# Kernel optimization log

Hardware: AMD Instinct MI355X
Metric: run time of the kernel (lower is better)

The kernel has to match this reference:

```python
import jax, jax.numpy as jnp
import numpy as np

B, N, M = 4, 1024, 1024
PFD, AD, GFD = 1024, 256, 512
H, DH = 4, 64
NR, CUT = 16, 2.0
SCALE = DH ** -0.5
OFFSETS = jnp.linspace(0.0, CUT, NR)
COEFF = -0.5 / (CUT / (NR - 1)) ** 2


def _ln(x, g, b, eps=1e-5):
    mu = x.mean(-1, keepdims=True)
    var = ((x - mu) ** 2).mean(-1, keepdims=True)
    return (x - mu) / jnp.sqrt(var + eps) * g + b


def _kabsch(src, tgt, w):
    # weighted Kabsch: rotation/translation aligning src -> tgt
    w = w / (w.sum(-1, keepdims=True) + 1e-8)  # (B,N)
    cs = jnp.einsum('bn,bnc->bc', w, src)
    ct = jnp.einsum('bn,bnc->bc', w, tgt)
    sc = src - cs[:, None]
    tc = tgt - ct[:, None]
    Hm = jnp.einsum('bn,bnc,bnd->bcd', w, sc, tc)  # (B,3,3)
    U, _, Vt = jnp.linalg.svd(Hm)
    V = jnp.swapaxes(Vt, -1, -2)
    d = jnp.linalg.det(V @ jnp.swapaxes(U, -1, -2))
    D = jnp.stack([jnp.ones_like(d), jnp.ones_like(d), d], -1)  # (B,3)
    R = jnp.einsum('bij,bj,bkj->bik', V, D, U)
    t = ct - jnp.einsum('bij,bj->bi', R, cs)
    return R, t


def setup_inputs():
    key = jax.random.key(0)
    it = iter(jax.random.split(key, 48))
    nrm = lambda s, sc=1.0: jax.random.normal(next(it), s, jnp.float32) * sc
    return {
        'src_point_feats': nrm((B, N, PFD)),
        'tgt_point_feats': nrm((B, M, PFD)),
        'src_points': nrm((B, N, 3)),
        'tgt_points': nrm((B, M, 3)),
        'tgt_global': nrm((B, GFD)),
        'sfp_w': nrm((PFD, AD), 0.02), 'sfp_b': jnp.zeros((AD,)), 'sfp_g': jnp.ones((AD,)), 'sfp_bb': jnp.zeros((AD,)),
        'tfp_w': nrm((PFD, AD), 0.02), 'tfp_b': jnp.zeros((AD,)), 'tfp_g': jnp.ones((AD,)), 'tfp_bb': jnp.zeros((AD,)),
        'rbf_w': nrm((NR, H), 0.1),
        'qw': nrm((AD, AD), 0.02), 'qb': jnp.zeros((AD,)),
        'kw': nrm((AD, AD), 0.02), 'kb': jnp.zeros((AD,)),
        'vw': nrm((AD, AD), 0.02), 'vb': jnp.zeros((AD,)),
        'ow': nrm((AD, AD), 0.02), 'ob': jnp.zeros((AD,)),
        'n1_g': jnp.ones((AD,)), 'n1_b': jnp.zeros((AD,)),
        'f1_w': nrm((AD, 4 * AD), 0.02), 'f1_b': jnp.zeros((4 * AD,)),
        'f2_w': nrm((4 * AD, AD), 0.02), 'f2_b': jnp.zeros((AD,)),
        'n2_g': jnp.ones((AD,)), 'n2_b': jnp.zeros((AD,)),
        'scp_w': nrm((AD, AD), 0.02), 'scp_b': jnp.zeros((AD,)),
        'tcp_w': nrm((AD, AD), 0.02), 'tcp_b': jnp.zeros((AD,)),
        'temperature': jnp.array(0.05, jnp.float32),
        'gp_w': nrm((AD, GFD), 0.02), 'gp_b': jnp.zeros((GFD,)), 'gp_g': jnp.ones((GFD,)), 'gp_bb': jnp.zeros((GFD,)),
    }


def reference(src_point_feats, tgt_point_feats, src_points, tgt_points, tgt_global,
              sfp_w, sfp_b, sfp_g, sfp_bb, tfp_w, tfp_b, tfp_g, tfp_bb, rbf_w,
              qw, qb, kw, kb, vw, vb, ow, ob, n1_g, n1_b,
              f1_w, f1_b, f2_w, f2_b, n2_g, n2_b,
              scp_w, scp_b, tcp_w, tcp_b, temperature,
              gp_w, gp_b, gp_g, gp_bb):
    # feature projections
    src_proj = jax.nn.relu(_ln(src_point_feats @ sfp_w + sfp_b, sfp_g, sfp_bb))  # (B,N,AD)
    tgt_proj = jax.nn.relu(_ln(tgt_point_feats @ tfp_w + tfp_b, tfp_g, tfp_bb))  # (B,M,AD)
    # inter-cloud geometric bias: cdist -> gaussian RBF -> per-head linear (dist no-grad)
    d2 = ((src_points ** 2).sum(-1)[:, :, None] + (tgt_points ** 2).sum(-1)[:, None, :]
          - 2.0 * jnp.einsum('bnc,bmc->bnm', src_points, tgt_points))
    dist = jnp.sqrt(jnp.clip(d2, 0.0))  # (B,N,M)
    rbf = jnp.exp(COEFF * (dist[..., None] - OFFSETS) ** 2)  # (B,N,M,NR)
    rbf = jax.lax.stop_gradient(rbf)
    bias = jnp.einsum('bnmr,rh->bhnm', rbf, rbf_w)
    # cross attention with geo bias (pre-LN on both streams, shared LN params)
    xq = _ln(src_proj, n1_g, n1_b)
    xc = _ln(tgt_proj, n1_g, n1_b)
    q = (xq @ qw + qb).reshape(B, N, H, DH)
    k = (xc @ kw + kb).reshape(B, M, H, DH)
    v = (xc @ vw + vb).reshape(B, M, H, DH)
    logits = jnp.einsum('bnhd,bmhd->bhnm', q, k) * SCALE + bias
    p = jax.nn.softmax(logits, axis=-1)
    attn_out = jnp.einsum('bhnm,bmhd->bnhd', p, v).reshape(B, N, AD) @ ow + ob
    x = src_proj + attn_out
    # FFN block (exact GELU as in torch)
    h = _ln(x, n2_g, n2_b)
    x = x + (jax.nn.gelu(h @ f1_w + f1_b, approximate=False) @ f2_w + f2_b)
    # soft correspondences + 3-step log-domain Sinkhorn
    src_corr = x @ scp_w + scp_b
    tgt_corr = tgt_proj @ tcp_w + tcp_b
    tau = jnp.clip(temperature, 0.01, 1.0)
    logS = jnp.einsum('bnd,bmd->bnm', src_corr, tgt_corr) / tau
    for _ in range(3):
        logS = logS - jax.nn.logsumexp(logS, axis=-1, keepdims=True)
        logS = logS - jax.nn.logsumexp(logS, axis=-2, keepdims=True)
    S = jnp.exp(logS)
    tgt_corr_points = jnp.einsum('bnm,bmc->bnc', S, tgt_points)
    confidence = S.max(-1)
    R_res, t_res = _kabsch(src_points, tgt_corr_points, confidence)
    src_global_new = jax.nn.relu(_ln(x.max(1) @ gp_w + gp_b, gp_g, gp_bb))
    combined = jnp.concatenate([src_global_new, tgt_global], axis=-1)
    return R_res, t_res, combined, confidence, S
```

## Files before the change

### kernel.cpp

```cpp
#include <hip/hip_runtime.h>
#include <hip/hip_bf16.h>
#include <math.h>

constexpr int Bn  = 4;
constexpr int Nn  = 1024;
constexpr int Mmm = 1024;
constexpr int PFDc = 1024;
constexpr int ADc  = 256;
constexpr int GFDc = 512;
constexpr int Hc   = 4;
constexpr int NRc  = 16;
constexpr int NSPLIT = 32;
constexpr float COEFFc = -28.125f;
constexpr float SCALEc = 0.125f;
constexpr float STEPc  = 2.0f / 15.0f;

__device__ __forceinline__ float addf(float a, float b) { return a + b; }
__device__ __forceinline__ double addd(double a, double b) { return a + b; }

#define BLK_REDUCE_F(OP, VAR, RES) \
  red[tid] = (VAR); __syncthreads(); \
  for (int st_ = 128; st_ > 0; st_ >>= 1) { if (tid < st_) red[tid] = OP(red[tid], red[tid + st_]); __syncthreads(); } \
  (RES) = red[0]; __syncthreads();

#define BLK_REDUCE_D(OP, VAR, RES) \
  redd[tid] = (VAR); __syncthreads(); \
  for (int st_ = 128; st_ > 0; st_ >>= 1) { if (tid < st_) redd[tid] = OP(redd[tid], redd[tid + st_]); __syncthreads(); } \
  (RES) = redd[0]; __syncthreads();

__global__ __launch_bounds__(256) void gemm_k(
    const float* __restrict__ A, const float* __restrict__ W, const float* __restrict__ bias,
    const float* __restrict__ addsrc, float* __restrict__ C,
    int R, int K, int Cc, int act)
{
  __shared__ __align__(16) float As[16][68];
  __shared__ __align__(16) float Ws[16][68];
  const int tid = threadIdx.x;
  const int tx = tid & 15, ty = tid >> 4;
  const int r0 = blockIdx.y * 64, c0 = blockIdx.x * 64;
  float acc[4][4] = {};
  for (int k0 = 0; k0 < K; k0 += 16) {
    #pragma unroll
    for (int j = 0; j < 4; ++j) {
      int e = tid + j * 256;
      int ar = e >> 4, ak = e & 15;
      int gr = r0 + ar;
      As[ak][ar] = (gr < R) ? A[(size_t)gr * K + k0 + ak] : 0.f;
    }
    #pragma unroll
    for (int j = 0; j < 4; ++j) {
      int e = tid + j * 256;
      int wk = e >> 6, wc = e & 63;
      int gc = c0 + wc;
      Ws[wk][wc] = (gc < Cc) ? W[(size_t)(k0 + wk) * Cc + gc] : 0.f;
    }
    __syncthreads();
    #pragma unroll
    for (int kk = 0; kk < 16; ++kk) {
      float4 av = *(const float4*)&As[kk][ty * 4];
      float4 wv = *(const float4*)&Ws[kk][tx * 4];
      float a[4] = {av.x, av.y, av.z, av.w};
      float w[4] = {wv.x, wv.y, wv.z, wv.w};
      #pragma unroll
      for (int i = 0; i < 4; ++i)
        #pragma unroll
        for (int j = 0; j < 4; ++j)
          acc[i][j] = fmaf(a[i], w[j], acc[i][j]);
    }
    __syncthreads();
  }
  #pragma unroll
  for (int i = 0; i < 4; ++i) {
    int r = r0 + ty * 4 + i;
    if (r >= R) continue;
    #pragma unroll
    for (int j = 0; j < 4; ++j) {
      int c = c0 + tx * 4 + j;
      if (c >= Cc) continue;
      float v = acc[i][j] + bias[c];
      if (addsrc) v += addsrc[(size_t)r * Cc + c];
      if (act == 1) v = 0.5f * v * (1.f + erff(v * 0.70710678118654752f));
      C[(size_t)r * Cc + c] = v;
    }
  }
}

__global__ __launch_bounds__(256) void gemm256_k(
    const float* __restrict__ A, const float* __restrict__ W, const float* __restrict__ bias,
    const float* __restrict__ addsrc, float* __restrict__ C,
    int R, int K, int Cc, int act)
{
  __shared__ __align__(16) float As[2][16][68];
  __shared__ __align__(16) float Ws[2][16][68];
  const int tid = threadIdx.x;
  const int tx = tid & 15, ty = tid >> 4;
  const int r0 = blockIdx.y * 64, c0 = blockIdx.x * 64;
  float acc[4][4] = {};
  float ra[4], rb[4];

  #pragma unroll
  for (int j = 0; j < 4; ++j) {
    int e = tid + j * 256;
    ra[j] = A[(size_t)(r0 + (e >> 4)) * K + (e & 15)];
    rb[j] = W[(size_t)(e >> 6) * Cc + c0 + (e & 63)];
  }
  #pragma unroll
  for (int j = 0; j < 4; ++j) {
    int e = tid + j * 256;
    As[0][e & 15][e >> 4] = ra[j];
    Ws[0][e >> 6][e & 63] = rb[j];
  }
  __syncthreads();

  const int nstep = K >> 4;
  for (int s = 0; s < nstep; ++s) {
    const int cur = s & 1;
    if (s + 1 < nstep) {
      const int k0 = (s + 1) << 4;
      #pragma unroll
      for (int j = 0; j < 4; ++j) {
        int e = tid + j * 256;
        ra[j] = A[(size_t)(r0 + (e >> 4)) * K + k0 + (e & 15)];
        rb[j] = W[(size_t)(k0 + (e >> 6)) * Cc + c0 + (e & 63)];
      }
    }
    #pragma unroll
    for (int kk = 0; kk < 16; ++kk) {
      float4 av = *(const float4*)&As[cur][kk][ty * 4];
      float4 wv = *(const float4*)&Ws[cur][kk][tx * 4];
      float a[4] = {av.x, av.y, av.z, av.w};
      float w[4] = {wv.x, wv.y, wv.z, wv.w};
      #pragma unroll
      for (int i = 0; i < 4; ++i)
        #pragma unroll
        for (int j = 0; j < 4; ++j)
          acc[i][j] = fmaf(a[i], w[j], acc[i][j]);
    }
    if (s + 1 < nstep) {
      #pragma unroll
      for (int j = 0; j < 4; ++j) {
        int e = tid + j * 256;
        As[cur ^ 1][e & 15][e >> 4] = ra[j];
        Ws[cur ^ 1][e >> 6][e & 63] = rb[j];
      }
    }
    __syncthreads();
  }
  #pragma unroll
  for (int i = 0; i < 4; ++i) {
    int r = r0 + ty * 4 + i;
    #pragma unroll
    for (int j = 0; j < 4; ++j) {
      int c = c0 + tx * 4 + j;
      float v = acc[i][j] + bias[c];
      if (addsrc) v += addsrc[(size_t)r * Cc + c];
      if (act == 1) v = 0.5f * v * (1.f + erff(v * 0.70710678118654752f));
      C[(size_t)r * Cc + c] = v;
    }
  }
}

__global__ __launch_bounds__(256) void gemm_sk_k(
    const float* __restrict__ A, const float* __restrict__ W, float* __restrict__ P)
{
  __shared__ __align__(16) float As[2][16][68];
  __shared__ __align__(16) float Ws[2][16][68];
  const int tid = threadIdx.x;
  const int tx = tid & 15, ty = tid >> 4;
  const int r0 = blockIdx.y * 64, c0 = blockIdx.x * 64;
  const int koff = blockIdx.z * 256;
  float acc[4][4] = {};
  float ra[4], rb[4];

  #pragma unroll
  for (int j = 0; j < 4; ++j) {
    int e = tid + j * 256;
    ra[j] = A[(size_t)(r0 + (e >> 4)) * 1024 + koff + (e & 15)];
    rb[j] = W[(size_t)(koff + (e >> 6)) * 256 + c0 + (e & 63)];
  }
  #pragma unroll
  for (int j = 0; j < 4; ++j) {
    int e = tid + j * 256;
    As[0][e & 15][e >> 4] = ra[j];
    Ws[0][e >> 6][e & 63] = rb[j];
  }
  __syncthreads();

  for (int s = 0; s < 16; ++s) {
    const int cur = s & 1;
    if (s + 1 < 16) {
      const int k0 = koff + ((s + 1) << 4);
      #pragma unroll
      for (int j = 0; j < 4; ++j) {
        int e = tid + j * 256;
        ra[j] = A[(size_t)(r0 + (e >> 4)) * 1024 + k0 + (e & 15)];
        rb[j] = W[(size_t)(k0 + (e >> 6)) * 256 + c0 + (e & 63)];
      }
    }
    #pragma unroll
    for (int kk = 0; kk < 16; ++kk) {
      float4 av = *(const float4*)&As[cur][kk][ty * 4];
      float4 wv = *(const float4*)&Ws[cur][kk][tx * 4];
      float a[4] = {av.x, av.y, av.z, av.w};
      float w[4] = {wv.x, wv.y, wv.z, wv.w};
      #pragma unroll
      for (int i = 0; i < 4; ++i)
        #pragma unroll
        for (int j = 0; j < 4; ++j)
          acc[i][j] = fmaf(a[i], w[j], acc[i][j]);
    }
    if (s + 1 < 16) {
      #pragma unroll
      for (int j = 0; j < 4; ++j) {
        int e = tid + j * 256;
        As[cur ^ 1][e & 15][e >> 4] = ra[j];
        Ws[cur ^ 1][e >> 6][e & 63] = rb[j];
      }
    }
    __syncthreads();
  }
  float* Pz = P + (size_t)blockIdx.z * 1048576;
  #pragma unroll
  for (int i = 0; i < 4; ++i) {
    int r = r0 + ty * 4 + i;
    #pragma unroll
    for (int j = 0; j < 4; ++j)
      Pz[(size_t)r * 256 + c0 + tx * 4 + j] = acc[i][j];
  }
}

__global__ __launch_bounds__(256) void ln4_k(
    const float* __restrict__ p, const float* __restrict__ bias,
    const float* __restrict__ g, const float* __restrict__ bb,
    float* __restrict__ out, int relu)
{
  const int row = blockIdx.x;
  const int tid = threadIdx.x;
  size_t o = (size_t)row * 256 + tid;
  float x = p[o] + p[o + 1048576] + p[o + 2097152] + p[o + 3145728] + bias[tid];
  float s = x, s2 = x * x;
  #pragma unroll
  for (int off = 32; off > 0; off >>= 1) {
    s  += __shfl_xor(s, off, 64);
    s2 += __shfl_xor(s2, off, 64);
  }
  __shared__ float as_[4], as2_[4];
  const int wv = tid >> 6, ln = tid & 63;
  if (ln == 0) { as_[wv] = s; as2_[wv] = s2; }
  __syncthreads();
  s  = as_[0] + as_[1] + as_[2] + as_[3];
  s2 = as2_[0] + as2_[1] + as2_[2] + as2_[3];
  float mu = s * (1.f / 256.f);
  float var = fmaxf(s2 * (1.f / 256.f) - mu * mu, 0.f);
  float inv = 1.f / sqrtf(var + 1e-5f);
  float v = (x - mu) * inv * g[tid] + bb[tid];
  if (relu) v = fmaxf(v, 0.f);
  out[o] = v;
}

__global__ __launch_bounds__(256) void red4_k(
    const float* __restrict__ p, const float* __restrict__ bias, float* __restrict__ out)
{
  size_t i = (size_t)blockIdx.x * 256 + threadIdx.x;
  out[i] += p[i] + p[i + 1048576] + p[i + 2097152] + p[i + 3145728] + bias[threadIdx.x];
}

__global__ __launch_bounds__(256) void pack_kv_k(
    const float* __restrict__ kw, const float* __restrict__ kb,
    const float* __restrict__ vw, const float* __restrict__ vb,
    float* __restrict__ kvw, float* __restrict__ kvb)
{
  int i = blockIdx.x * 256 + threadIdx.x;
  if (i < 256 * 512) {
    int r = i >> 9, c = i & 511;
    kvw[i] = (c < 256) ? kw[r * 256 + c] : vw[r * 256 + (c - 256)];
  } else if (i < 256 * 512 + 512) {
    int c = i - 256 * 512;
    kvb[c] = (c < 256) ? kb[c] : vb[c - 256];
  }
}

__global__ __launch_bounds__(256) void gemm_nt256_k(
    const float* __restrict__ A, const float* __restrict__ Bm, float* __restrict__ C,
    const float* __restrict__ temp)
{
  const int K = ADc;
  __shared__ __align__(16) float As[2][16][68];
  __shared__ __align__(16) float Bs[2][16][68];
  const int tid = threadIdx.x;
  const int tx = tid & 15, ty = tid >> 4;
  const int b = blockIdx.z;
  const int r0 = blockIdx.y * 64, c0 = blockIdx.x * 64;
  const float* Ab = A + (size_t)b * Nn * K;
  const float* Bb = Bm + (size_t)b * Mmm * K;
  float* Cb = C + (size_t)b * Nn * Mmm;
  float tau = fminf(fmaxf(temp[0], 0.01f), 1.0f);
  float inv_tau = 1.f / tau;
  float acc[4][4] = {};
  float ra[4], rb[4];

  #pragma unroll
  for (int j = 0; j < 4; ++j) {
    int e = tid + j * 256;
    ra[j] = Ab[(size_t)(r0 + (e >> 4)) * K + (e & 15)];
    rb[j] = Bb[(size_t)(c0 + (e >> 4)) * K + (e & 15)];
  }
  #pragma unroll
  for (int j = 0; j < 4; ++j) {
    int e = tid + j * 256;
    As[0][e & 15][e >> 4] = ra[j];
    Bs[0][e & 15][e >> 4] = rb[j];
  }
  __syncthreads();

  for (int s = 0; s < 16; ++s) {
    const int cur = s & 1;
    if (s + 1 < 16) {
      const int k0 = (s + 1) << 4;
      #pragma unroll
      for (int j = 0; j < 4; ++j) {
        int e = tid + j * 256;
        ra[j] = Ab[(size_t)(r0 + (e >> 4)) * K + k0 + (e & 15)];
        rb[j] = Bb[(size_t)(c0 + (e >> 4)) * K + k0 + (e & 15)];
      }
    }
    #pragma unroll
    for (int kk = 0; kk < 16; ++kk) {
      float4 av = *(const float4*)&As[cur][kk][ty * 4];
      float4 wv = *(const float4*)&Bs[cur][kk][tx * 4];
      float a[4] = {av.x, av.y, av.z, av.w};
      float w[4] = {wv.x, wv.y, wv.z, wv.w};
      #pragma unroll
      for (int i = 0; i < 4; ++i)
        #pragma unroll
        for (int j = 0; j < 4; ++j)
          acc[i][j] = fmaf(a[i], w[j], acc[i][j]);
    }
    if (s + 1 < 16) {
      #pragma unroll
      for (int j = 0; j < 4; ++j) {
        int e = tid + j * 256;
        As[cur ^ 1][e & 15][e >> 4] = ra[j];
        Bs[cur ^ 1][e & 15][e >> 4] = rb[j];
      }
    }
    __syncthreads();
  }
  #pragma unroll
  for (int i = 0; i < 4; ++i) {
    int r = r0 + ty * 4 + i;
    #pragma unroll
    for (int j = 0; j < 4; ++j) {
      int c = c0 + tx * 4 + j;
      Cb[(size_t)r * Mmm + c] = acc[i][j] * inv_tau;
    }
  }
}

__global__ __launch_bounds__(256) void ln_k(
    const float* __restrict__ in, const float* __restrict__ g, const float* __restrict__ bb,
    float* __restrict__ out, int Cc, int relu)
{
  const int tid = threadIdx.x;
  const int row = blockIdx.x;
  const float* x = in + (size_t)row * Cc;
  float* o = out + (size_t)row * Cc;
  __shared__ float red[256];
  float s = 0.f;
  for (int j = tid; j < Cc; j += 256) s += x[j];
  float tot; BLK_REDUCE_F(addf, s, tot);
  float mu = tot / Cc;
  float s2 = 0.f;
  for (int j = tid; j < Cc; j += 256) { float d = x[j] - mu; s2 += d * d; }
  float tot2; BLK_REDUCE_F(addf, s2, tot2);
  float inv = 1.f / sqrtf(tot2 / Cc + 1e-5f);
  for (int j = tid; j < Cc; j += 256) {
    float v = (x[j] - mu) * inv * g[j] + bb[j];
    if (relu) v = fmaxf(v, 0.f);
    o[j] = v;
  }
}

__global__ __launch_bounds__(256) void ln2_k(
    const float* __restrict__ in, const float* __restrict__ g, const float* __restrict__ bb,
    float* __restrict__ out, int relu)
{
  const int row = blockIdx.x;
  const int tid = threadIdx.x;
  float x = in[(size_t)row * 256 + tid];
  float s = x, s2 = x * x;
  #pragma unroll
  for (int off = 32; off > 0; off >>= 1) {
    s  += __shfl_xor(s, off, 64);
    s2 += __shfl_xor(s2, off, 64);
  }
  __shared__ float as_[4], as2_[4];
  const int wv = tid >> 6, ln = tid & 63;
  if (ln == 0) { as_[wv] = s; as2_[wv] = s2; }
  __syncthreads();
  s  = as_[0] + as_[1] + as_[2] + as_[3];
  s2 = as2_[0] + as2_[1] + as2_[2] + as2_[3];
  float mu = s * (1.f / 256.f);
  float var = fmaxf(s2 * (1.f / 256.f) - mu * mu, 0.f);
  float inv = 1.f / sqrtf(var + 1e-5f);
  float v = (x - mu) * inv * g[tid] + bb[tid];
  if (relu) v = fmaxf(v, 0.f);
  out[(size_t)row * 256 + tid] = v;
}

__global__ __launch_bounds__(256) void fattn(
    const float* __restrict__ q, const float* __restrict__ kv,
    const float* __restrict__ src_pts, const float* __restrict__ tgt_pts,
    const float* __restrict__ rbfw, float* __restrict__ ctx)
{
  const int bh = blockIdx.x;
  const int b = bh >> 2, h = bh & 3;
  const int n0 = blockIdx.y * 32;
  const int tid = threadIdx.x;
  const int tx = tid & 15, ty = tid >> 4;
  const int lane = tid & 63, w = tid >> 6;
  const int mml = lane >> 4;
  const int dd  = lane & 15;

  __shared__ __align__(16) float Qs[64][36];
  __shared__ __align__(16) float Ks[64][68];
  __shared__ __align__(16) float Vs[64][68];
  __shared__ __align__(16) float Ps[32][68];
  __shared__ float spx[32], spy[32], spz[32];
  __shared__ float tpx[64], tpy[64], tpz[64];
  __shared__ float rw[16];
  __shared__ float Tb[2048];

  if (tid < 16) rw[tid] = rbfw[tid * Hc + h];
  #pragma unroll
  for (int c = 0; c < 8; ++c) {
    int n = c * 4 + mml;
    int d = w * 16 + dd;
    Qs[d][n] = q[((size_t)b * Nn + n0 + n) * ADc + h * 64 + d];
  }
  if (tid < 32) {
    spx[tid] = src_pts[((size_t)b * Nn + n0 + tid) * 3 + 0];
    spy[tid] = src_pts[((size_t)b * Nn + n0 + tid) * 3 + 1];
    spz[tid] = src_pts[((size_t)b * Nn + n0 + tid) * 3 + 2];
  }
  __syncthreads();

  for (int i = tid; i < 2048; i += 256) {
    float di = (float)i * (1.0f / 512.0f);
    float s = 0.f;
    #pragma unroll
    for (int r = 0; r < NRc; ++r) {
      float dq = di - STEPc * r;
      s = fmaf(__expf(COEFFc * dq * dq), rw[r], s);
    }
    Tb[i] = s;
  }

  float kreg[16], vreg[16];
  float tp0 = 0.f, tp1 = 0.f, tp2 = 0.f;
  {
    const size_t kb_ = ((size_t)b * Mmm) * 512 + h * 64;
    #pragma unroll
    for (int c = 0; c < 16; ++c) {
      kreg[c] = kv[kb_ + (size_t)(c * 4 + mml) * 512 + w * 16 + dd];
      vreg[c] = kv[kb_ + (size_t)(c * 4 + w) * 512 + 256 + lane];
    }
    if (tid < 64) {
      tp0 = tgt_pts[((size_t)b * Mmm + tid) * 3 + 0];
      tp1 = tgt_pts[((size_t)b * Mmm + tid) * 3 + 1];
      tp2 = tgt_pts[((size_t)b * Mmm + tid) * 3 + 2];
    }
  }

  float O[2][4] = {};
  float mrun[2] = {-1e30f, -1e30f};
  float lrun[2] = {0.f, 0.f};

  for (int t = 0; t < Mmm / 64; ++t) {
    __syncthreads();
    #pragma unroll
    for (int c = 0; c < 16; ++c) Ks[w * 16 + dd][c * 4 + mml] = kreg[c];
    #pragma unroll
    for (int c = 0; c < 16; ++c) Vs[c * 4 + w][lane] = vreg[c];
    if (tid < 64) { tpx[tid] = tp0; tpy[tid] = tp1; tpz[tid] = tp2; }
    if (t + 1 < Mmm / 64) {
      const size_t kb_ = ((size_t)b * Mmm + (t + 1) * 64) * 512 + h * 64;
      #pragma unroll
      for (int c = 0; c < 16; ++c) {
        kreg[c] = kv[kb_ + (size_t)(c * 4 + mml) * 512 + w * 16 + dd];
        vreg[c] = kv[kb_ + (size_t)(c * 4 + w) * 512 + 256 + lane];
      }
      if (tid < 64) {
        size_t tb_ = ((size_t)b * Mmm + (t + 1) * 64 + tid) * 3;
        tp0 = tgt_pts[tb_ + 0];
        tp1 = tgt_pts[tb_ + 1];
        tp2 = tgt_pts[tb_ + 2];
      }
    }
    __syncthreads();

    float S[2][4] = {};
    #pragma unroll
    for (int d = 0; d < 64; ++d) {
      float2 qv = *(const float2*)&Qs[d][ty * 2];
      float4 kv4 = *(const float4*)&Ks[d][tx * 4];
      float kwv[4] = {kv4.x, kv4.y, kv4.z, kv4.w};
      #pragma unroll
      for (int j = 0; j < 4; ++j) {
        S[0][j] = fmaf(qv.x, kwv[j], S[0][j]);
        S[1][j] = fmaf(qv.y, kwv[j], S[1][j]);
      }
    }

    #pragma unroll
    for (int i = 0; i < 2; ++i) {
      int n = ty * 2 + i;
      float s0 = spx[n], s1 = spy[n], s2 = spz[n];
      float sq = s0 * s0 + s1 * s1 + s2 * s2;
      float rmx = -1e30f;
      #pragma unroll
      for (int j = 0; j < 4; ++j) {
        int mj = tx * 4 + j;
        float t0 = tpx[mj], t1 = tpy[mj], t2 = tpz[mj];
        float d2 = sq + t0 * t0 + t1 * t1 + t2 * t2 - 2.f * (s0 * t0 + s1 * t1 + s2 * t2);
        float dist = sqrtf(fmaxf(d2, 0.f));
        float fidx = fminf(dist * 512.0f, 2047.0f);
        int i0 = (int)fidx;
        i0 = (i0 > 2046) ? 2046 : i0;
        float frac = fidx - (float)i0;
        float b0 = Tb[i0];
        float bias = fmaf(Tb[i0 + 1] - b0, frac, b0);
        float lv = S[i][j] * SCALEc + bias;
        S[i][j] = lv;
        rmx = fmaxf(rmx, lv);
      }
      #pragma unroll
      for (int off = 1; off < 16; off <<= 1)
        rmx = fmaxf(rmx, __shfl_xor(rmx, off, 64));
      float mn = fmaxf(mrun[i], rmx);
      float alpha = __expf(mrun[i] - mn);
      mrun[i] = mn;
      float p0 = __expf(S[i][0] - mn);
      float p1 = __expf(S[i][1] - mn);
      float p2 = __expf(S[i][2] - mn);
      float p3 = __expf(S[i][3] - mn);
      *(float4*)&Ps[n][tx * 4] = make_float4(p0, p1, p2, p3);
      float rs = p0 + p1 + p2 + p3;
      #pragma unroll
      for (int off = 1; off < 16; off <<= 1)
        rs += __shfl_xor(rs, off, 64);
      lrun[i] = lrun[i] * alpha + rs;
      O[i][0] *= alpha; O[i][1] *= alpha; O[i][2] *= alpha; O[i][3] *= alpha;
    }

    #pragma unroll
    for (int m = 0; m < 64; ++m) {
      float4 vv = *(const float4*)&Vs[m][tx * 4];
      float vwv[4] = {vv.x, vv.y, vv.z, vv.w};
      float p0 = Ps[ty * 2][m];
      float p1 = Ps[ty * 2 + 1][m];
      #pragma unroll
      for (int j = 0; j < 4; ++j) {
        O[0][j] = fmaf(p0, vwv[j], O[0][j]);
        O[1][j] = fmaf(p1, vwv[j], O[1][j]);
      }
    }
  }

  #pragma unroll
  for (int i = 0; i < 2; ++i) {
    int n = n0 + ty * 2 + i;
    float invl = 1.f / lrun[i];
    size_t base = ((size_t)b * Nn + n) * ADc + h * 64 + tx * 4;
    ctx[base + 0] = O[i][0] * invl;
    ctx[base + 1] = O[i][1] * invl;
    ctx[base + 2] = O[i][2] * invl;
    ctx[base + 3] = O[i][3] * invl;
  }
}

__global__ __launch_bounds__(256) void row_lse2_k(float* __restrict__ logS, const float* __restrict__ colLse)
{
  const int tid = threadIdx.x;
  const int bn = blockIdx.x;
  const int b = bn >> 10;
  float* row = logS + (size_t)bn * Mmm;
  float4 v4 = *(float4*)&row[tid * 4];
  if (colLse) {
    const float4 c4 = *(const float4*)&colLse[(size_t)b * Mmm + tid * 4];
    v4.x -= c4.x; v4.y -= c4.y; v4.z -= c4.z; v4.w -= c4.w;
  }
  float mx = fmaxf(fmaxf(v4.x, v4.y), fmaxf(v4.z, v4.w));
  float sm = __expf(v4.x - mx) + __expf(v4.y - mx) + __expf(v4.z - mx) + __expf(v4.w - mx);
  #pragma unroll
  for (int off = 32; off > 0; off >>= 1) {
    float mo = __shfl_xor(mx, off, 64);
    float so = __shfl_xor(sm, off, 64);
    float mn = fmaxf(mx, mo);
    sm = sm * __expf(mx - mn) + so * __expf(mo - mn);
    mx = mn;
  }
  __shared__ float wm[4], wsum[4];
  const int wv = tid >> 6, ln = tid & 63;
  if (ln == 0) { wm[wv] = mx; wsum[wv] = sm; }
  __syncthreads();
  float m0 = fmaxf(fmaxf(wm[0], wm[1]), fmaxf(wm[2], wm[3]));
  float stot = wsum[0] * __expf(wm[0] - m0) + wsum[1] * __expf(wm[1] - m0)
             + wsum[2] * __expf(wm[2] - m0) + wsum[3] * __expf(wm[3] - m0);
  float lse = m0 + __logf(stot);
  v4.x -= lse; v4.y -= lse; v4.z -= lse; v4.w -= lse;
  *(float4*)&row[tid * 4] = v4;
}

__global__ __launch_bounds__(256) void col_part_k(
    const float* __restrict__ logS, float* __restrict__ pmax, float* __restrict__ psum)
{
  const int b = blockIdx.z, sp = blockIdx.y;
  const int m = blockIdx.x * 256 + threadIdx.x;
  const int RPS = Nn / NSPLIT;
  const float* base = logS + ((size_t)b * Nn + sp * RPS) * Mmm + m;
  float mx = -1e30f, sm = 0.f;
  for (int i = 0; i < RPS; ++i) {
    float v = base[(size_t)i * Mmm];
    if (v > mx) { sm = sm * __expf(mx - v) + 1.f; mx = v; }
    else sm += __expf(v - mx);
  }
  size_t o = ((size_t)b * NSPLIT + sp) * Mmm + m;
  pmax[o] = mx; psum[o] = sm;
}

__global__ __launch_bounds__(256) void col_comb_k(
    const float* __restrict__ pmax, const float* __restrict__ psum, float* __restrict__ colLse)
{
  const int b = blockIdx.y;
  const int m = blockIdx.x * 256 + threadIdx.x;
  float mx = -1e30f;
  for (int s = 0; s < NSPLIT; ++s) mx = fmaxf(mx, pmax[((size_t)b * NSPLIT + s) * Mmm + m]);
  float sm = 0.f;
  for (int s = 0; s < NSPLIT; ++s) {
    size_t o = ((size_t)b * NSPLIT + s) * Mmm + m;
    sm += psum[o] * __expf(pmax[o] - mx);
  }
  colLse[(size_t)b * Mmm + m] = mx + __logf(sm);
}

__global__ __launch_bounds__(256) void finalize_k(
    const float* __restrict__ logS, const float* __restrict__ colLse,
    const float* __restrict__ tgt_pts, float* __restrict__ outS, float* __restrict__ outConf,
    float* __restrict__ conf, float* __restrict__ tcp)
{
  const int tid = threadIdx.x;
  const int bn = blockIdx.x;
  const int b = bn >> 10;
  const float* row = logS + (size_t)bn * Mmm;
  const float* cl = colLse + (size_t)b * Mmm;
  const float* tp = tgt_pts + (size_t)b * Mmm * 3;
  __shared__ float red[256];
  float mx = -1e30f, s0 = 0.f, s1 = 0.f, s2 = 0.f;
  for (int m = tid; m < Mmm; m += 256) {
    float sv = __expf(row[m] - cl[m]);
    outS[(size_t)bn * Mmm + m] = sv;
    mx = fmaxf(mx, sv);
    s0 = fmaf(sv, tp[m * 3 + 0], s0);
    s1 = fmaf(sv, tp[m * 3 + 1], s1);
    s2 = fmaf(sv, tp[m * 3 + 2], s2);
  }
  float rmx, r0, r1, r2;
  BLK_REDUCE_F(fmaxf, mx, rmx);
  BLK_REDUCE_F(addf, s0, r0);
  BLK_REDUCE_F(addf, s1, r1);
  BLK_REDUCE_F(addf, s2, r2);
  if (tid == 0) {
    conf[bn] = rmx;
    outConf[bn] = rmx;
    tcp[(size_t)bn * 3 + 0] = r0;
    tcp[(size_t)bn * 3 + 1] = r1;
    tcp[(size_t)bn * 3 + 2] = r2;
  }
}

__global__ __launch_bounds__(256) void kabsch_red_k(
    const float* __restrict__ conf, const float* __restrict__ src_pts,
    const float* __restrict__ tcp, double* __restrict__ kab)
{
  const int b = blockIdx.x;
  const int tid = threadIdx.x;
  __shared__ double redd[256];
  __shared__ double sh[8];
  const float* cb = conf + (size_t)b * Nn;
  const float* sb = src_pts + (size_t)b * Nn * 3;
  const float* tb = tcp + (size_t)b * Nn * 3;

  double a = 0.0;
  for (int n = tid; n < Nn; n += 256) a += (double)cb[n];
  double wsum; BLK_REDUCE_D(addd, a, wsum);
  double inv = 1.0 / (wsum + 1e-8);

  double c0 = 0, c1 = 0, c2 = 0, t0 = 0, t1 = 0, t2 = 0;
  for (int n = tid; n < Nn; n += 256) {
    double wn = (double)cb[n] * inv;
    c0 += wn * (double)sb[n * 3 + 0];
    c1 += wn * (double)sb[n * 3 + 1];
    c2 += wn * (double)sb[n * 3 + 2];
    t0 += wn * (double)tb[n * 3 + 0];
    t1 += wn * (double)tb[n * 3 + 1];
    t2 += wn * (double)tb[n * 3 + 2];
  }
  double r;
  BLK_REDUCE_D(addd, c0, r); if (tid == 0) sh[0] = r; __syncthreads();
  BLK_REDUCE_D(addd, c1, r); if (tid == 0) sh[1] = r; __syncthreads();
  BLK_REDUCE_D(addd, c2, r); if (tid == 0) sh[2] = r; __syncthreads();
  BLK_REDUCE_D(addd, t0, r); if (tid == 0) sh[3] = r; __syncthreads();
  BLK_REDUCE_D(addd, t1, r); if (tid == 0) sh[4] = r; __syncthreads();
  BLK_REDUCE_D(addd, t2, r); if (tid == 0) sh[5] = r; __syncthreads();
  double cs[3] = {sh[0], sh[1], sh[2]};
  double ct[3] = {sh[3], sh[4], sh[5]};

  double hm[9] = {};
  for (int n = tid; n < Nn; n += 256) {
    double wn = (double)cb[n] * inv;
    double d0 = (double)sb[n * 3 + 0] - cs[0];
    double d1 = (double)sb[n * 3 + 1] - cs[1];
    double d2 = (double)sb[n * 3 + 2] - cs[2];
    double e0 = (double)tb[n * 3 + 0] - ct[0];
    double e1 = (double)tb[n * 3 + 1] - ct[1];
    double e2 = (double)tb[n * 3 + 2] - ct[2];
    hm[0] += wn * d0 * e0; hm[1] += wn * d0 * e1; hm[2] += wn * d0 * e2;
    hm[3] += wn * d1 * e0; hm[4] += wn * d1 * e1; hm[5] += wn * d1 * e2;
    hm[6] += wn * d2 * e0; hm[7] += wn * d2 * e1; hm[8] += wn * d2 * e2;
  }
  for (int i = 0; i < 9; ++i) {
    BLK_REDUCE_D(addd, hm[i], r);
    if (tid == 0) kab[(size_t)b * 16 + i] = r;
    __syncthreads();
  }
  if (tid == 0) {
    for (int i = 0; i < 3; ++i) {
      kab[(size_t)b * 16 + 9 + i]  = cs[i];
      kab[(size_t)b * 16 + 12 + i] = ct[i];
    }
  }
}

// ... 112 lines not shown
  const int b = blockIdx.x, ch = blockIdx.y;
  const int d = threadIdx.x;
  float mx = -1e30f;
  const int n0 = ch * 64;
  for (int n = n0; n < n0 + 64; ++n)
    mx = fmaxf(mx, x[((size_t)b * Nn + n) * ADc + d]);
  part[((size_t)b * 16 + ch) * ADc + d] = mx;
}

__global__ __launch_bounds__(256) void xmax_comb_k(const float* __restrict__ part, float* __restrict__ xmax)
{
  const int b = blockIdx.x, d = threadIdx.x;
  float mx = -1e30f;
  for (int c = 0; c < 16; ++c) mx = fmaxf(mx, part[((size_t)b * 16 + c) * ADc + d]);
  xmax[(size_t)b * ADc + d] = mx;
}

__global__ __launch_bounds__(256) void combined_k(
    const float* __restrict__ gl, const float* __restrict__ tgt_global, float* __restrict__ outC)
{
  int i = blockIdx.x * 256 + threadIdx.x;
  int b = i >> 10, j = i & 1023;
  float v = (j < GFDc) ? gl[(size_t)b * GFDc + j] : tgt_global[(size_t)b * GFDc + (j - GFDc)];
  outC[i] = v;
}

extern "C" void kernel_launch(void* const* d_in, const int* in_sizes, int n_in,
                              void* d_out, int out_size, void* d_ws, size_t ws_size,
                              hipStream_t stream) {
  (void)in_sizes; (void)n_in; (void)out_size; (void)ws_size;
  const float* src_feats = (const float*)d_in[0];
  const float* tgt_feats = (const float*)d_in[1];
  const float* src_pts   = (const float*)d_in[2];
  const float* tgt_pts   = (const float*)d_in[3];
  const float* tgt_glob  = (const float*)d_in[4];
  const float* sfp_w = (const float*)d_in[5];  const float* sfp_b = (const float*)d_in[6];
  const float* sfp_g = (const float*)d_in[7];  const float* sfp_bb = (const float*)d_in[8];
  const float* tfp_w = (const float*)d_in[9];  const float* tfp_b = (const float*)d_in[10];
  const float* tfp_g = (const float*)d_in[11]; const float* tfp_bb = (const float*)d_in[12];
  const float* rbf_w = (const float*)d_in[13];
  const float* qw = (const float*)d_in[14]; const float* qb = (const float*)d_in[15];
  const float* kw = (const float*)d_in[16]; const float* kb = (const float*)d_in[17];
  const float* vw = (const float*)d_in[18]; const float* vb = (const float*)d_in[19];
  const float* ow = (const float*)d_in[20]; const float* ob = (const float*)d_in[21];
  const float* n1_g = (const float*)d_in[22]; const float* n1_b = (const float*)d_in[23];
  const float* f1_w = (const float*)d_in[24]; const float* f1_b = (const float*)d_in[25];
  const float* f2_w = (const float*)d_in[26]; const float* f2_b = (const float*)d_in[27];
  const float* n2_g = (const float*)d_in[28]; const float* n2_b = (const float*)d_in[29];
  const float* scp_w = (const float*)d_in[30]; const float* scp_b = (const float*)d_in[31];
  const float* tcp_w = (const float*)d_in[32]; const float* tcp_b = (const float*)d_in[33];
  const float* temp  = (const float*)d_in[34];
  const float* gp_w = (const float*)d_in[35]; const float* gp_b = (const float*)d_in[36];
  const float* gp_g = (const float*)d_in[37]; const float* gp_bb = (const float*)d_in[38];

  float* out = (float*)d_out;
  float* outR    = out;
  float* outT    = out + 36;
  float* outC    = out + 48;
  float* outConf = out + 48 + 4096;
  float* outS    = out + 48 + 4096 + 4096;

  float* ws = (float*)d_ws;
  const size_t M1 = 1048576;
  float* A_   = ws + 0 * M1;
  float* B_   = ws + 1 * M1;
  float* C_   = ws + 2 * M1;
  float* D_   = ws + 3 * M1;
  float* E_   = ws + 4 * M1;
  float* F_   = ws + 5 * M1;
  float* G_   = ws + 6 * M1;
  float* logS = ws + 0 * M1;
  float* hid  = ws + 1 * M1;
  float* tail = ws + 7 * M1;
  float* colLse = tail;
  float* pmax   = colLse + 4096;
  float* psum   = pmax + 131072;
  float* conf   = psum + 131072;
  float* tcp    = conf + 4096;
  float* xmax   = tcp + 12288;
  float* glraw  = xmax + 1024;
  float* gl     = glraw + 2048;
  double* kab   = (double*)(gl + 2048);
  float* xpart  = (float*)(kab + 64);
  float* kvw    = pmax;
  float* kvb    = psum;

  const int BN = Bn * Nn;

  pack_kv_k<<<514, 256, 0, stream>>>(kw, kb, vw, vb, kvw, kvb);

  gemm_sk_k<<<dim3(4, 64, 4), 256, 0, stream>>>(src_feats, sfp_w, outS);
  ln4_k<<<BN, 256, 0, stream>>>(outS, sfp_b, sfp_g, sfp_bb, G_, 1);
  gemm_sk_k<<<dim3(4, 64, 4), 256, 0, stream>>>(tgt_feats, tfp_w, outS);
  ln4_k<<<BN, 256, 0, stream>>>(outS, tfp_b, tfp_g, tfp_bb, F_, 1);

  ln2_k<<<BN, 256, 0, stream>>>(G_, n1_g, n1_b, A_, 0);
  gemm256_k<<<dim3(4, 64), 256, 0, stream>>>(A_, qw, qb, nullptr, C_, BN, ADc, ADc, 0);
  ln2_k<<<BN, 256, 0, stream>>>(F_, n1_g, n1_b, B_, 0);
  gemm256_k<<<dim3(8, 64), 256, 0, stream>>>(B_, kvw, kvb, nullptr, D_, BN, ADc, 512, 0);

  fattn<<<dim3(Bn * Hc, Nn / 32), 256, 0, stream>>>(C_, D_, src_pts, tgt_pts, rbf_w, B_);
  gemm256_k<<<dim3(4, 64), 256, 0, stream>>>(B_, ow, ob, G_, G_, BN, ADc, ADc, 0);

  ln2_k<<<BN, 256, 0, stream>>>(G_, n2_g, n2_b, A_, 0);
  gemm256_k<<<dim3(16, 64), 256, 0, stream>>>(A_, f1_w, f1_b, nullptr, hid, BN, ADc, 1024, 1);
  gemm_sk_k<<<dim3(4, 64, 4), 256, 0, stream>>>(hid, f2_w, outS);
  red4_k<<<BN, 256, 0, stream>>>(outS, f2_b, G_);

  gemm256_k<<<dim3(4, 64), 256, 0, stream>>>(G_, scp_w, scp_b, nullptr, E_, BN, ADc, ADc, 0);

  xmax_part_k<<<dim3(Bn, 16), 256, 0, stream>>>(G_, xpart);
  xmax_comb_k<<<Bn, 256, 0, stream>>>(xpart, xmax);
  gemm_k<<<dim3(GFDc / 64, 1), 256, 0, stream>>>(xmax, gp_w, gp_b, nullptr, glraw, Bn, ADc, GFDc, 0);
  ln_k<<<Bn, 256, 0, stream>>>(glraw, gp_g, gp_bb, gl, GFDc, 1);
  combined_k<<<(Bn * 2 * GFDc) / 256, 256, 0, stream>>>(gl, tgt_glob, outC);

  gemm256_k<<<dim3(4, 64), 256, 0, stream>>>(F_, tcp_w, tcp_b, nullptr, G_, BN, ADc, ADc, 0);
  gemm_nt256_k<<<dim3(16, 16, Bn), 256, 0, stream>>>(E_, G_, logS, temp);

  for (int it = 0; it < 3; ++it) {
    row_lse2_k<<<BN, 256, 0, stream>>>(logS, it == 0 ? nullptr : colLse);
    col_part_k<<<dim3(Mmm / 256, NSPLIT, Bn), 256, 0, stream>>>(logS, pmax, psum);
    col_comb_k<<<dim3(Mmm / 256, Bn), 256, 0, stream>>>(pmax, psum, colLse);
  }
  finalize_k<<<BN, 256, 0, stream>>>(logS, colLse, tgt_pts, outS, outConf, conf, tcp);

  kabsch_red_k<<<Bn, 256, 0, stream>>>(conf, src_pts, tcp, kab);
  kabsch_svd_k<<<1, 64, 0, stream>>>(kab, outR, outT);
}
```

Measured before the change: 743.2 us.

## Use 512-thread GEMMs, fuse LN and corr projections, defer Sinkhorn row normalization

Several GEMMs move to a new 512-thread, 64x64-tile core with 2x4 outputs per thread, giving more waves per block. The two n1 layernorms and the two correspondence projections are each merged into one launch. The Sinkhorn row pass now writes only a per-row logsumexp vector instead of rewriting the full logS matrix, and the column pass and finalize subtract it on the fly, saving a full read-modify-write of the 4x1024x1024 matrix per iteration. The attention bias table stores value and delta as a float2 so interpolation needs one load. Costs are smaller per-thread register tiles in the GEMMs and an extra global read in the column pass.

Measured after the change: 741.8 us. No clear change (-0.2%).

```diff
diff --git a/kernel.cpp b/kernel.cpp
--- a/kernel.cpp
+++ b/kernel.cpp
@@ -28,6 +28,138 @@
   for (int st_ = 128; st_ > 0; st_ >>= 1) { if (tid < st_) redd[tid] = OP(redd[tid], redd[tid + st_]); __syncthreads(); } \
   (RES) = redd[0]; __syncthreads();
 
+__device__ __forceinline__ void g512core(
+    const float* __restrict__ A, int lda, const float* __restrict__ W, int ldw,
+    int kbeg, int kend, int r0, int c0, int tid,
+    float As[2][16][68], float Ws[2][16][68], float acc[2][4])
+{
+  const int tx = tid & 15, ty = tid >> 4;
+  float ra[2], rb[2];
+  #pragma unroll
+  for (int j = 0; j < 2; ++j) {
+    int e = tid + j * 512;
+    ra[j] = A[(size_t)(r0 + (e >> 4)) * lda + kbeg + (e & 15)];
+    rb[j] = W[(size_t)(kbeg + (e >> 6)) * ldw + c0 + (e & 63)];
+  }
+  #pragma unroll
+  for (int j = 0; j < 2; ++j) {
+    int e = tid + j * 512;
+    As[0][e & 15][e >> 4] = ra[j];
+    Ws[0][e >> 6][e & 63] = rb[j];
+  }
+  __syncthreads();
+
+  const int nstep = (kend - kbeg) >> 4;
+  for (int s = 0; s < nstep; ++s) {
+    const int cur = s & 1;
+    if (s + 1 < nstep) {
+      const int k0 = kbeg + ((s + 1) << 4);
+      #pragma unroll
+      for (int j = 0; j < 2; ++j) {
+        int e = tid + j * 512;
+        ra[j] = A[(size_t)(r0 + (e >> 4)) * lda + k0 + (e & 15)];
+        rb[j] = W[(size_t)(k0 + (e >> 6)) * ldw + c0 + (e & 63)];
+      }
+    }
+    #pragma unroll
+    for (int kk = 0; kk < 16; ++kk) {
+      float2 av = *(const float2*)&As[cur][kk][ty * 2];
+      float4 wv = *(const float4*)&Ws[cur][kk][tx * 4];
+      float a[2] = {av.x, av.y};
+      float w[4] = {wv.x, wv.y, wv.z, wv.w};
+      #pragma unroll
+      for (int i = 0; i < 2; ++i)
+        #pragma unroll
+        for (int j = 0; j < 4; ++j)
+          acc[i][j] = fmaf(a[i], w[j], acc[i][j]);
+    }
+    if (s + 1 < nstep) {
+      #pragma unroll
+      for (int j = 0; j < 2; ++j) {
+        int e = tid + j * 512;
+        As[cur ^ 1][e & 15][e >> 4] = ra[j];
+        Ws[cur ^ 1][e >> 6][e & 63] = rb[j];
+      }
+    }
+    __syncthreads();
+  }
+}
+
+__global__ __launch_bounds__(512) void gemm512_k(
+    const float* __restrict__ A, const float* __restrict__ W, const float* __restrict__ bias,
+    const float* __restrict__ addsrc, float* __restrict__ C,
+    int K, int Cc, int act)
+{
+  __shared__ __align__(16) float As[2][16][68];
+  __shared__ __align__(16) float Ws[2][16][68];
+  const int tid = threadIdx.x;
+  const int tx = tid & 15, ty = tid >> 4;
+  const int r0 = blockIdx.y * 64, c0 = blockIdx.x * 64;
+  float acc[2][4] = {};
+  g512core(A, K, W, Cc, 0, K, r0, c0, tid, As, Ws, acc);
+  #pragma unroll
+  for (int i = 0; i < 2; ++i) {
+    int r = r0 + ty * 2 + i;
+    #pragma unroll
+    for (int j = 0; j < 4; ++j) {
+      int c = c0 + tx * 4 + j;
+      float v = acc[i][j] + bias[c];
+      if (addsrc) v += addsrc[(size_t)r * Cc + c];
+      if (act == 1) v = 0.5f * v * (1.f + erff(v * 0.70710678118654752f));
+      C[(size_t)r * Cc + c] = v;
+    }
+  }
+}
+
+__global__ __launch_bounds__(512) void gemm_sk512_k(
+    const float* __restrict__ A, const float* __restrict__ W, float* __restrict__ P)
+{
+  __shared__ __align__(16) float As[2][16][68];
+  __shared__ __align__(16) float Ws[2][16][68];
+  const int tid = threadIdx.x;
+  const int tx = tid & 15, ty = tid >> 4;
+  const int r0 = blockIdx.y * 64, c0 = blockIdx.x * 64;
+  const int koff = blockIdx.z * 256;
+  float acc[2][4] = {};
+  g512core(A, 1024, W, 256, koff, koff + 256, r0, c0, tid, As, Ws, acc);
+  float* Pz = P + (size_t)blockIdx.z * 1048576;
+  #pragma unroll
+  for (int i = 0; i < 2; ++i) {
+    int r = r0 + ty * 2 + i;
+    #pragma unroll
+    for (int j = 0; j < 4; ++j)
+      Pz[(size_t)r * 256 + c0 + tx * 4 + j] = acc[i][j];
+  }
+}
+
+__global__ __launch_bounds__(512) void gemm_corr2_k(
+    const float* __restrict__ A0, const float* __restrict__ W0, const float* __restrict__ b0,
+    float* __restrict__ C0,
+    const float* __restrict__ A1, const float* __restrict__ W1, const float* __restrict__ b1,
+    float* __restrict__ C1)
+{
+  __shared__ __align__(16) float As[2][16][68];
+  __shared__ __align__(16) float Ws[2][16][68];
+  const int tid = threadIdx.x;
+  const int tx = tid & 15, ty = tid >> 4;
+  const int r0 = blockIdx.y * 64, c0 = blockIdx.x * 64;
+  const float* A = blockIdx.z ? A1 : A0;
+  const float* W = blockIdx.z ? W1 : W0;
+  const float* bias = blockIdx.z ? b1 : b0;
+  float* C = blockIdx.z ? C1 : C0;
+  float acc[2][4] = {};
+  g512core(A, 256, W, 256, 0, 256, r0, c0, tid, As, Ws, acc);
+  #pragma unroll
+  for (int i = 0; i < 2; ++i) {
+    int r = r0 + ty * 2 + i;
+    #pragma unroll
+    for (int j = 0; j < 4; ++j) {
+      int c = c0 + tx * 4 + j;
+      C[(size_t)r * 256 + c] = acc[i][j] + bias[c];
+    }
+  }
+}
+
 __global__ __launch_bounds__(256) void gemm_k(
     const float* __restrict__ A, const float* __restrict__ W, const float* __restrict__ bias,
     const float* __restrict__ addsrc, float* __restrict__ C,
@@ -157,75 +289,6 @@
       if (act == 1) v = 0.5f * v * (1.f + erff(v * 0.70710678118654752f));
       C[(size_t)r * Cc + c] = v;
     }
-  }
-}
-
-__global__ __launch_bounds__(256) void gemm_sk_k(
-    const float* __restrict__ A, const float* __restrict__ W, float* __restrict__ P)
-{
-  __shared__ __align__(16) float As[2][16][68];
-  __shared__ __align__(16) float Ws[2][16][68];
-  const int tid = threadIdx.x;
-  const int tx = tid & 15, ty = tid >> 4;
-  const int r0 = blockIdx.y * 64, c0 = blockIdx.x * 64;
-  const int koff = blockIdx.z * 256;
-  float acc[4][4] = {};
-  float ra[4], rb[4];
-
-  #pragma unroll
-  for (int j = 0; j < 4; ++j) {
-    int e = tid + j * 256;
-    ra[j] = A[(size_t)(r0 + (e >> 4)) * 1024 + koff + (e & 15)];
-    rb[j] = W[(size_t)(koff + (e >> 6)) * 256 + c0 + (e & 63)];
-  }
-  #pragma unroll
-  for (int j = 0; j < 4; ++j) {
-    int e = tid + j * 256;
-    As[0][e & 15][e >> 4] = ra[j];
-    Ws[0][e >> 6][e & 63] = rb[j];
-  }
-  __syncthreads();
-
-  for (int s = 0; s < 16; ++s) {
-    const int cur = s & 1;
-    if (s + 1 < 16) {
-      const int k0 = koff + ((s + 1) << 4);
-      #pragma unroll
-      for (int j = 0; j < 4; ++j) {
-        int e = tid + j * 256;
-        ra[j] = A[(size_t)(r0 + (e >> 4)) * 1024 + k0 + (e & 15)];
-        rb[j] = W[(size_t)(k0 + (e >> 6)) * 256 + c0 + (e & 63)];
-      }
-    }
-    #pragma unroll
-    for (int kk = 0; kk < 16; ++kk) {
-      float4 av = *(const float4*)&As[cur][kk][ty * 4];
-      float4 wv = *(const float4*)&Ws[cur][kk][tx * 4];
-      float a[4] = {av.x, av.y, av.z, av.w};
-      float w[4] = {wv.x, wv.y, wv.z, wv.w};
-      #pragma unroll
-      for (int i = 0; i < 4; ++i)
-        #pragma unroll
-        for (int j = 0; j < 4; ++j)
-          acc[i][j] = fmaf(a[i], w[j], acc[i][j]);
-    }
-    if (s + 1 < 16) {
-      #pragma unroll
-      for (int j = 0; j < 4; ++j) {
-        int e = tid + j * 256;
-        As[cur ^ 1][e & 15][e >> 4] = ra[j];
-        Ws[cur ^ 1][e >> 6][e & 63] = rb[j];
-      }
-    }
-    __syncthreads();
-  }
-  float* Pz = P + (size_t)blockIdx.z * 1048576;
-  #pragma unroll
-  for (int i = 0; i < 4; ++i) {
-    int r = r0 + ty * 4 + i;
-    #pragma unroll
-    for (int j = 0; j < 4; ++j)
-      Pz[(size_t)r * 256 + c0 + tx * 4 + j] = acc[i][j];
   }
 }
 
@@ -381,12 +444,10 @@
   }
 }
 
-__global__ __launch_bounds__(256) void ln2_k(
+__device__ __forceinline__ void ln2_body(
     const float* __restrict__ in, const float* __restrict__ g, const float* __restrict__ bb,
-    float* __restrict__ out, int relu)
-{
-  const int row = blockIdx.x;
-  const int tid = threadIdx.x;
+    float* __restrict__ out, int row, int tid, int relu)
+{
   float x = in[(size_t)row * 256 + tid];
   float s = x, s2 = x * x;
   #pragma unroll
@@ -408,6 +469,23 @@
   out[(size_t)row * 256 + tid] = v;
 }
 
+__global__ __launch_bounds__(256) void ln2_k(
+    const float* __restrict__ in, const float* __restrict__ g, const float* __restrict__ bb,
+    float* __restrict__ out, int relu)
+{
+  ln2_body(in, g, bb, out, blockIdx.x, threadIdx.x, relu);
+}
+
+__global__ __launch_bounds__(256) void ln2x2_k(
+    const float* __restrict__ in0, float* __restrict__ out0,
+    const float* __restrict__ in1, float* __restrict__ out1,
+    const float* __restrict__ g, const float* __restrict__ bb)
+{
+  const int row = blockIdx.x;
+  if (row < Bn * Nn) ln2_body(in0, g, bb, out0, row, threadIdx.x, 0);
+  else               ln2_body(in1, g, bb, out1, row - Bn * Nn, threadIdx.x, 0);
+}
+
 __global__ __launch_bounds__(256) void fattn(
     const float* __restrict__ q, const float* __restrict__ kv,
     const float* __restrict__ src_pts, const float* __restrict__ tgt_pts,
@@ -429,7 +507,7 @@
   __shared__ float spx[32], spy[32], spz[32];
   __shared__ float tpx[64], tpy[64], tpz[64];
   __shared__ float rw[16];
-  __shared__ float Tb[2048];
+  __shared__ __align__(8) float2 Tb[2048];
 
   if (tid < 16) rw[tid] = rbfw[tid * Hc + h];
   #pragma unroll
@@ -447,13 +525,15 @@
 
   for (int i = tid; i < 2048; i += 256) {
     float di = (float)i * (1.0f / 512.0f);
-    float s = 0.f;
+    float s0 = 0.f, s1 = 0.f;
     #pragma unroll
     for (int r = 0; r < NRc; ++r) {
-      float dq = di - STEPc * r;
-      s = fmaf(__expf(COEFFc * dq * dq), rw[r], s);
-    }
-    Tb[i] = s;
+      float dq0 = di - STEPc * r;
+      float dq1 = dq0 + (1.0f / 512.0f);
+      s0 = fmaf(__expf(COEFFc * dq0 * dq0), rw[r], s0);
+      s1 = fmaf(__expf(COEFFc * dq1 * dq1), rw[r], s1);
+    }
+    Tb[i] = make_float2(s0, s1 - s0);
   }
 
   float kreg[16], vreg[16];
@@ -526,10 +606,9 @@
         float dist = sqrtf(fmaxf(d2, 0.f));
         float fidx = fminf(dist * 512.0f, 2047.0f);
         int i0 = (int)fidx;
-        i0 = (i0 > 2046) ? 2046 : i0;
         float frac = fidx - (float)i0;
-        float b0 = Tb[i0];
-        float bias = fmaf(Tb[i0 + 1] - b0, frac, b0);
+        float2 tb = Tb[i0];
+        float bias = fmaf(tb.y, frac, tb.x);
         float lv = S[i][j] * SCALEc + bias;
         S[i][j] = lv;
         rmx = fmaxf(rmx, lv);
@@ -579,15 +658,16 @@
   }
 }
 
-__global__ __launch_bounds__(256) void row_lse2_k(float* __restrict__ logS, const float* __restrict__ colLse)
+__global__ __launch_bounds__(256) void row_lse3_k(
+    const float* __restrict__ logS, const float* __restrict__ Cm, float* __restrict__ Rn)
 {
   const int tid = threadIdx.x;
   const int bn = blockIdx.x;
   const int b = bn >> 10;
-  float* row = logS + (size_t)bn * Mmm;
-  float4 v4 = *(float4*)&row[tid * 4];
-  if (colLse) {
-    const float4 c4 = *(const float4*)&colLse[(size_t)b * Mmm + tid * 4];
+  const float* row = logS + (size_t)bn * Mmm;
+  float4 v4 = *(const float4*)&row[tid * 4];
+  if (Cm) {
+    const float4 c4 = *(const float4*)&Cm[(size_t)b * Mmm + tid * 4];
     v4.x -= c4.x; v4.y -= c4.y; v4.z -= c4.z; v4.w -= c4.w;
   }
   float mx = fmaxf(fmaxf(v4.x, v4.y), fmaxf(v4.z, v4.w));
@@ -604,24 +684,26 @@
   const int wv = tid >> 6, ln = tid & 63;
   if (ln == 0) { wm[wv] = mx; wsum[wv] = sm; }
   __syncthreads();
-  float m0 = fmaxf(fmaxf(wm[0], wm[1]), fmaxf(wm[2], wm[3]));
-  float stot = wsum[0] * __expf(wm[0] - m0) + wsum[1] * __expf(wm[1] - m0)
-             + wsum[2] * __expf(wm[2] - m0) + wsum[3] * __expf(wm[3] - m0);
-  float lse = m0 + __logf(stot);
-  v4.x -= lse; v4.y -= lse; v4.z -= lse; v4.w -= lse;
-  *(float4*)&row[tid * 4] = v4;
-}
-
-__global__ __launch_bounds__(256) void col_part_k(
-    const float* __restrict__ logS, float* __restrict__ pmax, float* __restrict__ psum)
+  if (tid == 0) {
+    float m0 = fmaxf(fmaxf(wm[0], wm[1]), fmaxf(wm[2], wm[3]));
+    float stot = wsum[0] * __expf(wm[0] - m0) + wsum[1] * __expf(wm[1] - m0)
+               + wsum[2] * __expf(wm[2] - m0) + wsum[3] * __expf(wm[3] - m0);
+    Rn[bn] = m0 + __logf(stot);
+  }
+}
+
+__global__ __launch_bounds__(256) void col_part2_k(
+    const float* __restrict__ logS, const float* __restrict__ Rn,
+    float* __restrict__ pmax, float* __restrict__ psum)
 {
   const int b = blockIdx.z, sp = blockIdx.y;
   const int m = blockIdx.x * 256 + threadIdx.x;
   const int RPS = Nn / NSPLIT;
   const float* base = logS + ((size_t)b * Nn + sp * RPS) * Mmm + m;
+  const float* rn = Rn + (size_t)b * Nn + sp * RPS;
   float mx = -1e30f, sm = 0.f;
   for (int i = 0; i < RPS; ++i) {
-    float v = base[(size_t)i * Mmm];
+    float v = base[(size_t)i * Mmm] - rn[i];
     if (v > mx) { sm = sm * __expf(mx - v) + 1.f; mx = v; }
     else sm += __expf(v - mx);
   }
@@ -644,8 +726,8 @@
   colLse[(size_t)b * Mmm + m] = mx + __logf(sm);
 }
 
-__global__ __launch_bounds__(256) void finalize_k(
-    const float* __restrict__ logS, const float* __restrict__ colLse,
+__global__ __launch_bounds__(256) void finalize2_k(
+    const float* __restrict__ logS, const float* __restrict__ Rn, const float* __restrict__ Cm,
     const float* __restrict__ tgt_pts, float* __restrict__ outS, float* __restrict__ outConf,
     float* __restrict__ conf, float* __restrict__ tcp)
 {
@@ -653,12 +735,13 @@
   const int bn = blockIdx.x;
   const int b = bn >> 10;
   const float* row = logS + (size_t)bn * Mmm;
-  const float* cl = colLse + (size_t)b * Mmm;
+  const float rsub = Rn[bn];
+  const float* cl = Cm + (size_t)b * Mmm;
   const float* tp = tgt_pts + (size_t)b * Mmm * 3;
   __shared__ float red[256];
   float mx = -1e30f, s0 = 0.f, s1 = 0.f, s2 = 0.f;
   for (int m = tid; m < Mmm; m += 256) {
-    float sv = __expf(row[m] - cl[m]);
+    float sv = __expf(row[m] - rsub - cl[m]);
     outS[(size_t)bn * Mmm + m] = sv;
     mx = fmaxf(mx, sv);
     s0 = fmaf(sv, tp[m * 3 + 0], s0);
@@ -937,6 +1020,7 @@
   float* gl     = glraw + 2048;
   double* kab   = (double*)(gl + 2048);
   float* xpart  = (float*)(kab + 64);
+  float* Rn     = xpart + 16384;
   float* kvw    = pmax;
   float* kvb    = psum;
 
@@ -944,42 +1028,40 @@
 
   pack_kv_k<<<514, 256, 0, stream>>>(kw, kb, vw, vb, kvw, kvb);
 
-  gemm_sk_k<<<dim3(4, 64, 4), 256, 0, stream>>>(src_feats, sfp_w, outS);
+  gemm_sk512_k<<<dim3(4, 64, 4), 512, 0, stream>>>(src_feats, sfp_w, outS);
   ln4_k<<<BN, 256, 0, stream>>>(outS, sfp_b, sfp_g, sfp_bb, G_, 1);
-  gemm_sk_k<<<dim3(4, 64, 4), 256, 0, stream>>>(tgt_feats, tfp_w, outS);
+  gemm_sk512_k<<<dim3(4, 64, 4), 512, 0, stream>>>(tgt_feats, tfp_w, outS);
   ln4_k<<<BN, 256, 0, stream>>>(outS, tfp_b, tfp_g, tfp_bb, F_, 1);
 
-  ln2_k<<<BN, 256, 0, stream>>>(G_, n1_g, n1_b, A_, 0);
-  gemm256_k<<<dim3(4, 64), 256, 0, stream>>>(A_, qw, qb, nullptr, C_, BN, ADc, ADc, 0);
-  ln2_k<<<BN, 256, 0, stream>>>(F_, n1_g, n1_b, B_, 0);
-  gemm256_k<<<dim3(8, 64), 256, 0, stream>>>(B_, kvw, kvb, nullptr, D_, BN, ADc, 512, 0);
+  ln2x2_k<<<2 * BN, 256, 0, stream>>>(G_, A_, F_, B_, n1_g, n1_b);
+  gemm512_k<<<dim3(4, 64), 512, 0, stream>>>(A_, qw, qb, nullptr, C_, ADc, ADc, 0);
+  gemm512_k<<<dim3(8, 64), 512, 0, stream>>>(B_, kvw, kvb, nullptr, D_, ADc, 512, 0);
 
   fattn<<<dim3(Bn * Hc, Nn / 32), 256, 0, stream>>>(C_, D_, src_pts, tgt_pts, rbf_w, B_);
-  gemm256_k<<<dim3(4, 64), 256, 0, stream>>>(B_, ow, ob, G_, G_, BN, ADc, ADc, 0);
+  gemm512_k<<<dim3(4, 64), 512, 0, stream>>>(B_, ow, ob, G_, G_, ADc, ADc, 0);
 
   ln2_k<<<BN, 256, 0, stream>>>(G_, n2_g, n2_b, A_, 0);
   gemm256_k<<<dim3(16, 64), 256, 0, stream>>>(A_, f1_w, f1_b, nullptr, hid, BN, ADc, 1024, 1);
-  gemm_sk_k<<<dim3(4, 64, 4), 256, 0, stream>>>(hid, f2_w, outS);
+  gemm_sk512_k<<<dim3(4, 64, 4), 512, 0, stream>>>(hid, f2_w, outS);
   red4_k<<<BN, 256, 0, stream>>>(outS, f2_b, G_);
 
-  gemm256_k<<<dim3(4, 64), 256, 0, stream>>>(G_, scp_w, scp_b, nullptr, E_, BN, ADc, ADc, 0);
+  gemm_corr2_k<<<dim3(4, 64, 2), 512, 0, stream>>>(G_, scp_w, scp_b, E_,
+                                                   F_, tcp_w, tcp_b, outS);
+  gemm_nt256_k<<<dim3(16, 16, Bn), 256, 0, stream>>>(E_, outS, logS, temp);
+
+  for (int it = 0; it < 3; ++it) {
+    row_lse3_k<<<BN, 256, 0, stream>>>(logS, it == 0 ? nullptr : colLse, Rn);
+    col_part2_k<<<dim3(Mmm / 256, NSPLIT, Bn), 256, 0, stream>>>(logS, Rn, pmax, psum);
+    col_comb_k<<<dim3(Mmm / 256, Bn), 256, 0, stream>>>(pmax, psum, colLse);
+  }
+  finalize2_k<<<BN, 256, 0, stream>>>(logS, Rn, colLse, tgt_pts, outS, outConf, conf, tcp);
+
+  kabsch_red_k<<<Bn, 256, 0, stream>>>(conf, src_pts, tcp, kab);
+  kabsch_svd_k<<<1, 64, 0, stream>>>(kab, outR, outT);
 
   xmax_part_k<<<dim3(Bn, 16), 256, 0, stream>>>(G_, xpart);
   xmax_comb_k<<<Bn, 256, 0, stream>>>(xpart, xmax);
   gemm_k<<<dim3(GFDc / 64, 1), 256, 0, stream>>>(xmax, gp_w, gp_b, nullptr, glraw, Bn, ADc, GFDc, 0);
   ln_k<<<Bn, 256, 0, stream>>>(glraw, gp_g, gp_bb, gl, GFDc, 1);
   combined_k<<<(Bn * 2 * GFDc) / 256, 256, 0, stream>>>(gl, tgt_glob, outC);
-
-  gemm256_k<<<dim3(4, 64), 256, 0, stream>>>(F_, tcp_w, tcp_b, nullptr, G_, BN, ADc, ADc, 0);
-  gemm_nt256_k<<<dim3(16, 16, Bn), 256, 0, stream>>>(E_, G_, logS, temp);
-
-  for (int it = 0; it < 3; ++it) {
-    row_lse2_k<<<BN, 256, 0, stream>>>(logS, it == 0 ? nullptr : colLse);
-    col_part_k<<<dim3(Mmm / 256, NSPLIT, Bn), 256, 0, stream>>>(logS, pmax, psum);
-    col_comb_k<<<dim3(Mmm / 256, Bn), 256, 0, stream>>>(pmax, psum, colLse);
-  }
-  finalize_k<<<BN, 256, 0, stream>>>(logS, colLse, tgt_pts, outS, outConf, conf, tcp);
-
-  kabsch_red_k<<<Bn, 256, 0, stream>>>(conf, src_pts, tcp, kab);
-  kabsch_svd_k<<<1, 64, 0, stream>>>(kab, outR, outT);
-}
+}
```
